# Kernel tuning notes

Hardware: AMD Instinct MI355X
Metric: run time of the kernel (lower is better)

## Reference

```python
import jax, jax.numpy as jnp
import numpy as np

N = 50000            # nodes
E = 800000           # random edges (self loops added in reference, per PyG default)
D_IN, D1, D2, D_OUT = 256, 128, 64, 40
SLOPE = 0.2          # GATv2Conv default negative_slope


def _glorot(key, shape):
    fan_in, fan_out = shape[0], shape[-1]
    s = jnp.sqrt(6.0 / (fan_in + fan_out))
    return jax.random.uniform(key, shape, jnp.float32, -s, s)


def setup_inputs() -> dict:
    key = jax.random.key(0)
    ks = jax.random.split(key, 16)
    inp = {
        "x": jax.random.normal(ks[0], (N, D_IN), jnp.float32),
        "edge_index": jax.random.randint(ks[1], (2, E), 0, N),
    }
    dims = [(D_IN, D1), (D1, D2), (D2, D_OUT)]
    k = 2
    for i, (di, do) in enumerate(dims, 1):
        inp[f"W{i}l"] = _glorot(ks[k], (di, do)); k += 1
        inp[f"W{i}r"] = _glorot(ks[k], (di, do)); k += 1
        inp[f"b{i}l"] = jnp.zeros((do,), jnp.float32)
        inp[f"b{i}r"] = jnp.zeros((do,), jnp.float32)
        inp[f"a{i}"]  = _glorot(ks[k], (do,));    k += 1
        inp[f"c{i}"]  = jnp.zeros((do,), jnp.float32)
    return inp


def _gatv2(x, src, dst, Wl, bl, Wr, br, att, bias):
    # GATv2Conv, heads=1: lin_l on source nodes, lin_r on target nodes
    xl = x @ Wl + bl                     # [N, do] source transform
    xr = x @ Wr + br                     # [N, do] target transform
    e = jax.nn.leaky_relu(xl[src] + xr[dst], SLOPE)   # [Etot, do]
    logits = e @ att                     # [Etot]
    # segment softmax over incoming edges of each dst node
    m = jax.ops.segment_max(logits, dst, num_segments=N)
    ex = jnp.exp(logits - m[dst])
    denom = jax.ops.segment_sum(ex, dst, num_segments=N)
    alpha = ex / denom[dst]              # [Etot]
    out = jax.ops.segment_sum(alpha[:, None] * xl[src], dst, num_segments=N)
    return out + bias


def reference(x, edge_index,
              W1l, W1r, b1l, b1r, a1, c1,
              W2l, W2r, b2l, b2r, a2, c2,
              W3l, W3r, b3l, b3r, a3, c3):
    loop = jnp.arange(N, dtype=edge_index.dtype)
    src = jnp.concatenate([edge_index[0], loop])   # add_self_loops=True
    dst = jnp.concatenate([edge_index[1], loop])
    h = jax.nn.relu(_gatv2(x, src, dst, W1l, b1l, W1r, b1r, a1, c1))
    h = jax.nn.relu(_gatv2(h, src, dst, W2l, b2l, W2r, b2r, a2, c2))
    h = _gatv2(h, src, dst, W3l, b3l, W3r, b3r, a3, c3)
    return jax.nn.log_softmax(h, axis=1)
```

## Files before the change

### kernel.cpp

```cpp
#include <hip/hip_runtime.h>
#include <math.h>

#define NN 50000
#define NE 800000
#define SLOPE 0.2f
#define NEGX (-1e30f)
#define CH 8192

typedef _Float16 h8 __attribute__((ext_vector_type(8)));
typedef _Float16 h2 __attribute__((ext_vector_type(2)));
typedef float f8 __attribute__((ext_vector_type(8)));
typedef float v4f __attribute__((ext_vector_type(4)));

__device__ __forceinline__ h8 hzero(){ h8 z = {0,0,0,0,0,0,0,0}; return z; }
__device__ __forceinline__ f8 fzero(){ f8 z = {0,0,0,0,0,0,0,0}; return z; }

__device__ __forceinline__ void pack_one(const float* __restrict__ W,
                                         _Float16* __restrict__ Wp,
                                         int DO, int K, int NT, int t){
  int KC = K >> 5;
  if (t >= NT * KC * 64) return;
  int lane = t & 63;
  int rest = t >> 6;
  int c  = rest % KC;
  int nt = rest / KC;
  int col = nt * 16 + (lane & 15);
  int k0  = c * 32 + ((lane >> 4) << 3);
  _Float16 o[8];
#pragma unroll
  for (int j = 0; j < 8; j++){
    float v = (col < DO) ? W[(k0 + j) * DO + col] : 0.f;
    o[j] = (_Float16)v;
  }
  *(ulonglong2*)(Wp + (size_t)t * 8) = *(ulonglong2*)o;
}

__global__ __launch_bounds__(256) void k_pack_hist(
    const float* W1l, const float* W1r, const float* W2l,
    const float* W2r, const float* W3l, const float* W3r,
    _Float16* p1l, _Float16* p1r, _Float16* p2l,
    _Float16* p2r, _Float16* p3l, _Float16* p3r,
    const int* __restrict__ ei, int* __restrict__ gbp){
  __shared__ int h[256];
  int b = blockIdx.x, t = threadIdx.x;
  if (b < 44){
    if      (b < 16) pack_one(W1l, p1l, 128, 256, 8, (b     ) * 256 + t);
    else if (b < 32) pack_one(W1r, p1r, 128, 256, 8, (b - 16) * 256 + t);
    else if (b < 36) pack_one(W2l, p2l,  64, 128, 4, (b - 32) * 256 + t);
    else if (b < 40) pack_one(W2r, p2r,  64, 128, 4, (b - 36) * 256 + t);
    else if (b < 42) pack_one(W3l, p3l,  40,  64, 3, (b - 40) * 256 + t);
    else             pack_one(W3r, p3r,  40,  64, 3, (b - 42) * 256 + t);
  } else {
    int hb = b - 44;
    h[t] = 0;
    __syncthreads();
    int e0 = hb * 12500;
    for (int i = t; i < 12500; i += 256)
      atomicAdd(&h[ei[NE + e0 + i] >> 8], 1);
    __syncthreads();
    gbp[hb * 256 + t] = h[t];
  }
}

__global__ __launch_bounds__(256) void k_scan(const int* __restrict__ gbp,
                                              int* __restrict__ base,
                                              int* __restrict__ bcur,
                                              int* __restrict__ row_ptr){
  __shared__ int s[256];
  int t = threadIdx.x;
  int v = 0;
#pragma unroll 8
  for (int i = 0; i < 64; i++) v += gbp[i * 256 + t];
  s[t] = v; __syncthreads();
  for (int off = 1; off < 256; off <<= 1){
    int a = (t >= off) ? s[t - off] : 0;
    __syncthreads(); s[t] += a; __syncthreads();
  }
  int ex = s[t] - v;
  base[t] = ex;
  bcur[t] = ex;
  if (t == 255){ base[256] = s[255]; row_ptr[NN] = s[255]; }
}

__global__ __launch_bounds__(256) void k_bscatter(const int* __restrict__ ei,
                                                  int* __restrict__ bcur,
                                                  unsigned* __restrict__ pk_out){
  __shared__ unsigned pk[CH];
  __shared__ int h[256];
  int t = threadIdx.x;
  int e0 = blockIdx.x * CH;
  h[t] = 0;
  __syncthreads();
  int n = NE - e0; if (n > CH) n = CH;
  for (int i = t; i < n; i += 256){
    int e = e0 + i;
    int s = ei[e], d = ei[NE + e];
    pk[i] = (unsigned)s | ((unsigned)(d & 255) << 16) | ((unsigned)(d >> 8) << 24);
    atomicAdd(&h[d >> 8], 1);
  }
  __syncthreads();
  int c = h[t];
  if (c) h[t] = atomicAdd(&bcur[t], c);
  __syncthreads();
  for (int i = t; i < n; i += 256){
    unsigned u = pk[i];
    int pos = atomicAdd(&h[u >> 24], 1);
    pk_out[pos] = u;
  }
}

__global__ __launch_bounds__(256) void k_bcsr(const unsigned* __restrict__ pk,
                                              const int* __restrict__ base,
                                              int* __restrict__ row_ptr,
                                              int* __restrict__ csr_src){
  __shared__ int h[256], s[256];
  int t = threadIdx.x;
  int b = blockIdx.x;
  int lo = base[b], hi = base[b + 1];
  h[t] = 0;
  __syncthreads();
  for (int i = lo + t; i < hi; i += 256)
    atomicAdd(&h[(pk[i] >> 16) & 255], 1);
  __syncthreads();
  int v = h[t];
  s[t] = v; __syncthreads();
  for (int off = 1; off < 256; off <<= 1){
    int a = (t >= off) ? s[t - off] : 0;
    __syncthreads(); s[t] += a; __syncthreads();
  }
  int ex = lo + s[t] - v;
  int node = b * 256 + t;
  if (node < NN) row_ptr[node] = ex;
  h[t] = ex;
  __syncthreads();
  for (int i = lo + t; i < hi; i += 256){
    unsigned u = pk[i];
    int pos = atomicAdd(&h[(u >> 16) & 255], 1);
    csr_src[pos] = (int)(u & 0xFFFFu);
  }
}

template<typename TI, int K, int DO>
__global__ __launch_bounds__(256, 4) void gemm_direct(
    const TI* __restrict__ X,
    const _Float16* __restrict__ Wpl, const float* __restrict__ bl,
    const _Float16* __restrict__ Wpr, const float* __restrict__ br,
    _Float16* __restrict__ Yl, _Float16* __restrict__ Yr)
{
  constexpr int KC = K / 32;
  constexpr int NT = (DO + 15) / 16;
  int lane = threadIdx.x & 63;
  int wv   = threadIdx.x >> 6;
  int row0 = (blockIdx.x * 4 + wv) * 16;
  int arow = lane & 15;
  int koff = lane >> 4;
  int lrow = row0 + arow;
  int crow = (lrow < NN) ? lrow : 0;

  h8 afrag[KC];
  if constexpr (sizeof(TI) == 4){
    const float* Xr = (const float*)X + (size_t)crow * K + koff * 8;
#pragma unroll
    for (int c = 0; c < KC; c++){
      float4 v0 = *reinterpret_cast<const float4*>(Xr + c * 32);
      float4 v1 = *reinterpret_cast<const float4*>(Xr + c * 32 + 4);
      h8 a;
      a[0]=(_Float16)v0.x; a[1]=(_Float16)v0.y; a[2]=(_Float16)v0.z; a[3]=(_Float16)v0.w;
      a[4]=(_Float16)v1.x; a[5]=(_Float16)v1.y; a[6]=(_Float16)v1.z; a[7]=(_Float16)v1.w;
      afrag[c] = a;
    }
  } else {
    const _Float16* Xr = (const _Float16*)X + (size_t)crow * K + koff * 8;
#pragma unroll
    for (int c = 0; c < KC; c++)
      afrag[c] = *reinterpret_cast<const h8*>(Xr + c * 32);
  }

#pragma unroll
  for (int side = 0; side < 2; side++){
    const _Float16* Wp = side ? Wpr : Wpl;
    const float* bias = side ? br : bl;
    _Float16* Y = side ? Yr : Yl;
#pragma unroll
    for (int nt = 0; nt < NT; nt++){
      v4f acc = {0.f, 0.f, 0.f, 0.f};
#pragma unroll
      for (int c = 0; c < KC; c++){
        h8 b = *reinterpret_cast<const h8*>(Wp + (size_t)((nt * KC + c) * 64 + lane) * 8);
        acc = __builtin_amdgcn_mfma_f32_16x16x32_f16(afrag[c], b, acc, 0, 0, 0);
      }
      int col = nt * 16 + arow;
      if (col < DO){
        float bv = bias[col];
        int rbase = row0 + koff * 4;
#pragma unroll
        for (int r = 0; r < 4; r++){
          int orow = rbase + r;
          if (orow < NN) Y[(size_t)orow * DO + col] = (_Float16)(acc[r] + bv);
        }
      }
    }
  }
}

__device__ __forceinline__ float edge_logit(h8 x, h8 xrv, h8 attv){
  h8 t = x + xrv;
  h8 l = __builtin_elementwise_max(t, t * (_Float16)SLOPE);
  const h2* lp = (const h2*)&l;
  const h2* ap = (const h2*)&attv;
  h2 d = lp[0] * ap[0];
  d += lp[1] * ap[1];
  d += lp[2] * ap[2];
  d += lp[3] * ap[3];
  return (float)d[0] + (float)d[1];
}

template<int LPG>
__device__ __forceinline__ float gsum(float v){
#pragma unroll
  for (int off = 1; off < LPG; off <<= 1) v += __shfl_xor(v, off, 64);
  return v;
}
template<int LPG>
__device__ __forceinline__ void gsum2(float& a, float& b){
#pragma unroll
  for (int off = 1; off < LPG; off <<= 1){
    a += __shfl_xor(a, off, 64);
    b += __shfl_xor(b, off, 64);
  }
}
template<int LPG>
__device__ __forceinline__ void gsum4(float& a, float& b, float& c, float& d){
#pragma unroll
  for (int off = 1; off < LPG; off <<= 1){
    a += __shfl_xor(a, off, 64);
    b += __shfl_xor(b, off, 64);
    c += __shfl_xor(c, off, 64);
    d += __shfl_xor(d, off, 64);
  }
}
template<int LPG>
__device__ __forceinline__ float gmax(float v){
#pragma unroll
  for (int off = 1; off < LPG; off <<= 1) v = fmaxf(v, __shfl_xor(v, off, 64));
  return v;
}

template<int DO, int LPG, int DO2>
__global__ __launch_bounds__(256) void agg_gemm(
    const _Float16* __restrict__ xl, const _Float16* __restrict__ xr,
    const int* __restrict__ csr_src, const int* __restrict__ row_ptr,
    const float* __restrict__ att, const float* __restrict__ bias,
    const _Float16* __restrict__ Wpl2, const float* __restrict__ bl2,
    const _Float16* __restrict__ Wpr2, const float* __restrict__ br2,
    _Float16* __restrict__ Yl, _Float16* __restrict__ Yr)
{
  constexpr int G = 64 / LPG;
  constexpr int NPB = 4 * G;
  constexpr int LK = DO + 8;
  constexpr int KC2 = DO / 32;
  constexpr int NT2 = (DO2 + 15) / 16;
  constexpr int MT = NPB / 16;
  __shared__ _Float16 hs[NPB * LK];
  __shared__ int nodeOf[NPB];
  __shared__ int degOf[NPB];

  int tid  = threadIdx.x;
  int lane = tid & 63;
  int wid  = tid >> 6;

  if (tid < NPB){
    int nd = blockIdx.x * NPB + tid;
    degOf[tid] = (nd < NN) ? (row_ptr[nd + 1] - row_ptr[nd]) : -1;
  }
  __syncthreads();
  if (tid < NPB){
    int dg = degOf[tid];
    int r = 0;
#pragma unroll
    for (int j = 0; j < NPB; j++){
      int dj = degOf[j];
      r += (dj < dg) || (dj == dg && j < tid);
    }
    nodeOf[r] = blockIdx.x * NPB + tid;
  }
  __syncthreads();

  int g = lane / LPG, p = lane % LPG;
  int nodeLocal = wid * G + g;
  int node = nodeOf[nodeLocal];
  int cbase = p * 8;
  bool nvalid = node < NN;
  int nodeC = nvalid ? node : 0;

  h8 attv, xrv, xlv;
  {
    float4 a0 = *reinterpret_cast<const float4*>(att + cbase);
    float4 a1 = *reinterpret_cast<const float4*>(att + cbase + 4);
    attv[0]=(_Float16)a0.x; attv[1]=(_Float16)a0.y; attv[2]=(_Float16)a0.z; attv[3]=(_Float16)a0.w;
    attv[4]=(_Float16)a1.x; attv[5]=(_Float16)a1.y; attv[6]=(_Float16)a1.z; attv[7]=(_Float16)a1.w;
    xrv = *reinterpret_cast<const h8*>(xr + nodeC * DO + cbase);
    xlv = *reinterpret_cast<const h8*>(xl + nodeC * DO + cbase);
  }
  float s = gsum<LPG>(edge_logit(xlv, xrv, attv));
  float wS = __expf(s);
  float denA = wS, denB = 0.f;
  f8 accA, accB;
  {
    f8 xf = __builtin_convertvector(xlv, f8);
    accA = xf * wS;
    accB = fzero();
  }

  int e0 = row_ptr[nodeC];
  int e1 = nvalid ? row_ptr[nodeC + 1] : e0;
  int e = e0;
  for (; e + 3 < e1; e += 4){
    int s0 = csr_src[e],     s1 = csr_src[e + 1];
    int s2 = csr_src[e + 2], s3 = csr_src[e + 3];
    h8 x0 = *reinterpret_cast<const h8*>(xl + s0 * DO + cbase);
    h8 x1 = *reinterpret_cast<const h8*>(xl + s1 * DO + cbase);
    h8 x2 = *reinterpret_cast<const h8*>(xl + s2 * DO + cbase);
    h8 x3 = *reinterpret_cast<const h8*>(xl + s3 * DO + cbase);
    float p0 = edge_logit(x0, xrv, attv);
    float p1 = edge_logit(x1, xrv, attv);
    float p2 = edge_logit(x2, xrv, attv);
    float p3 = edge_logit(x3, xrv, attv);
    gsum4<LPG>(p0, p1, p2, p3);
    float w0 = __expf(p0), w1 = __expf(p1);
    float w2 = __expf(p2), w3 = __expf(p3);
    denA += w0 + w2; denB += w1 + w3;
    accA = __builtin_convertvector(x0, f8) * w0 + accA;
    accB = __builtin_convertvector(x1, f8) * w1 + accB;
    accA = __builtin_convertvector(x2, f8) * w2 + accA;
    accB = __builtin_convertvector(x3, f8) * w3 + accB;
  }
  for (; e + 1 < e1; e += 2){
    int sA = csr_src[e], sB = csr_src[e + 1];
    h8 xA = *reinterpret_cast<const h8*>(xl + sA * DO + cbase);
    h8 xB = *reinterpret_cast<const h8*>(xl + sB * DO + cbase);
    float pA = edge_logit(xA, xrv, attv);
    float pB = edge_logit(xB, xrv, attv);
    gsum2<LPG>(pA, pB);
    float wA = __expf(pA), wB = __expf(pB);
    denA += wA; denB += wB;
    accA = __builtin_convertvector(xA, f8) * wA + accA;
    accB = __builtin_convertvector(xB, f8) * wB + accB;
  }
  if (e < e1){
    int sA = csr_src[e];
    h8 xA = *reinterpret_cast<const h8*>(xl + sA * DO + cbase);
    float pA = gsum<LPG>(edge_logit(xA, xrv, attv));
    float w = __expf(pA);
    denA += w;
    accA = __builtin_convertvector(xA, f8) * w + accA;
  }

  {
    float inv = 1.0f / (denA + denB);
    f8 sum = (accA + accB) * inv;
    float4 b0 = *reinterpret_cast<const float4*>(bias + cbase);
    float4 b1 = *reinterpret_cast<const float4*>(bias + cbase + 4);
    f8 bv = {b0.x, b0.y, b0.z, b0.w, b1.x, b1.y, b1.z, b1.w};
    sum += bv;
    sum = __builtin_elementwise_max(sum, fzero());
    *reinterpret_cast<h8*>(&hs[nodeLocal * LK + cbase]) = __builtin_convertvector(sum, h8);
  }
  __syncthreads();

  int arow = lane & 15;
  int koff = lane >> 4;
  int mt = (MT == 1) ? 0 : (wid >> 1);
  h8 afrag[KC2];
#pragma unroll
  for (int c = 0; c < KC2; c++)
    afrag[c] = *reinterpret_cast<const h8*>(&hs[(mt * 16 + arow) * LK + koff * 8 + c * 32]);

  int side = wid & 1;
  const _Float16* Wp = side ? Wpr2 : Wpl2;
  const float* bias2 = side ? br2 : bl2;
  _Float16* Y = side ? Yr : Yl;
  int nt_begin = (MT == 1) ? (wid >> 1) * (NT2 / 2) : 0;
  int nt_end   = (MT == 1) ? nt_begin + NT2 / 2 : NT2;
  for (int nt = nt_begin; nt < nt_end; nt++){
    v4f acc = {0.f, 0.f, 0.f, 0.f};
#pragma unroll
    for (int c = 0; c < KC2; c++){
      h8 b = *reinterpret_cast<const h8*>(Wp + (size_t)((nt * KC2 + c) * 64 + lane) * 8);
      acc = __builtin_amdgcn_mfma_f32_16x16x32_f16(afrag[c], b, acc, 0, 0, 0);
    }
    int col = nt * 16 + arow;
    if (col < DO2){
      float bv = bias2[col];
      int lrbase = mt * 16 + koff * 4;
#pragma unroll
      for (int r = 0; r < 4; r++){
        int orow = nodeOf[lrbase + r];
        if (orow < NN) Y[(size_t)orow * DO2 + col] = (_Float16)(acc[r] + bv);
      }
    }
  }
}

template<int DO, int LPG>
__global__ __launch_bounds__(256) void gat_agg_out(
    const _Float16* __restrict__ xl, const _Float16* __restrict__ xr,
    const int* __restrict__ csr_src, const int* __restrict__ row_ptr,
    const float* __restrict__ att, const float* __restrict__ bias,
    float* __restrict__ out)
{
  constexpr int G = 64 / LPG;
  constexpr int NPB = 4 * G;
  __shared__ int nodeOf[NPB];
  __shared__ int degOf[NPB];
  int tid  = threadIdx.x;
  int lane = tid & 63;
  int wid  = tid >> 6;

  if (tid < NPB){
    int nd = blockIdx.x * NPB + tid;
    degOf[tid] = (nd < NN) ? (row_ptr[nd + 1] - row_ptr[nd]) : -1;
  }
  __syncthreads();
  if (tid < NPB){
    int dg = degOf[tid];
    int r = 0;
#pragma unroll
    for (int j = 0; j < NPB; j++){
      int dj = degOf[j];
      r += (dj < dg) || (dj == dg && j < tid);
    }
    nodeOf[r] = blockIdx.x * NPB + tid;
  }
  __syncthreads();

  int g = lane / LPG;
  int p = lane % LPG;
  int node = nodeOf[wid * G + g];
  bool nvalid = node < NN;
  int nodeC = nvalid ? node : 0;
  int cbase = p * 8;
  bool ok = (cbase < DO);

  h8 attv = hzero(), xrv = hzero(), xlv = hzero();
  if (ok){
    float4 a0 = *reinterpret_cast<const float4*>(att + cbase);
    float4 a1 = *reinterpret_cast<const float4*>(att + cbase + 4);
    attv[0]=(_Float16)a0.x; attv[1]=(_Float16)a0.y; attv[2]=(_Float16)a0.z; attv[3]=(_Float16)a0.w;
    attv[4]=(_Float16)a1.x; attv[5]=(_Float16)a1.y; attv[6]=(_Float16)a1.z; attv[7]=(_Float16)a1.w;
    xrv = *reinterpret_cast<const h8*>(xr + nodeC * DO + cbase);
    xlv = *reinterpret_cast<const h8*>(xl + nodeC * DO + cbase);
  }

  float s = gsum<LPG>(edge_logit(xlv, xrv, attv));
  float wS = __expf(s);
  float denA = wS, denB = 0.f;
  f8 accA, accB;
  {
    f8 xf = __builtin_convertvector(xlv, f8);
    accA = xf * wS;
    accB = fzero();
  }

  int e0 = row_ptr[nodeC];
  int e1 = nvalid ? row_ptr[nodeC + 1] : e0;
  int e = e0;
  for (; e + 3 < e1; e += 4){
    int s0 = csr_src[e],     s1 = csr_src[e + 1];
    int s2 = csr_src[e + 2], s3 = csr_src[e + 3];
    h8 x0 = ok ? *reinterpret_cast<const h8*>(xl + s0 * DO + cbase) : hzero();
    h8 x1 = ok ? *reinterpret_cast<const h8*>(xl + s1 * DO + cbase) : hzero();
    h8 x2 = ok ? *reinterpret_cast<const h8*>(xl + s2 * DO + cbase) : hzero();
    h8 x3 = ok ? *reinterpret_cast<const h8*>(xl + s3 * DO + cbase) : hzero();
    float p0 = edge_logit(x0, xrv, attv);
    float p1 = edge_logit(x1, xrv, attv);
    float p2 = edge_logit(x2, xrv, attv);
    float p3 = edge_logit(x3, xrv, attv);
    gsum4<LPG>(p0, p1, p2, p3);
    float w0 = __expf(p0), w1 = __expf(p1);
    float w2 = __expf(p2), w3 = __expf(p3);
    denA += w0 + w2; denB += w1 + w3;
    accA = __builtin_convertvector(x0, f8) * w0 + accA;
    accB = __builtin_convertvector(x1, f8) * w1 + accB;
    accA = __builtin_convertvector(x2, f8) * w2 + accA;
    accB = __builtin_convertvector(x3, f8) * w3 + accB;
  }
  for (; e + 1 < e1; e += 2){
    int sA = csr_src[e], sB = csr_src[e + 1];
    h8 xA = ok ? *reinterpret_cast<const h8*>(xl + sA * DO + cbase) : hzero();
    h8 xB = ok ? *reinterpret_cast<const h8*>(xl + sB * DO + cbase) : hzero();
    float pA = edge_logit(xA, xrv, attv);
    float pB = edge_logit(xB, xrv, attv);
    gsum2<LPG>(pA, pB);
    float wA = __expf(pA), wB = __expf(pB);
    denA += wA; denB += wB;
    accA = __builtin_convertvector(xA, f8) * wA + accA;
    accB = __builtin_convertvector(xB, f8) * wB + accB;
  }
  if (e < e1){
    int sA = csr_src[e];
    h8 xA = ok ? *reinterpret_cast<const h8*>(xl + sA * DO + cbase) : hzero();
    float pA = gsum<LPG>(edge_logit(xA, xrv, attv));
    float w = __expf(pA);
    denA += w;
    accA = __builtin_convertvector(xA, f8) * w + accA;
  }

  float inv = 1.0f / (denA + denB);
  f8 sumv = (accA + accB) * inv;
  float v[8]; float lmax = NEGX;
#pragma unroll
  for (int j = 0; j < 8; j++){
    v[j] = ok ? (sumv[j] + bias[cbase + j]) : NEGX;
    lmax = fmaxf(lmax, v[j]);
  }
  lmax = gmax<LPG>(lmax);
  float lsum = 0.f;
#pragma unroll
  for (int j = 0; j < 8; j++) lsum += __expf(v[j] - lmax);
  lsum = gsum<LPG>(lsum);
  if (ok && nvalid){
    float lg = lmax + __logf(lsum);
    float* op = (float*)out + node * DO + cbase;
    float4 o0, o1;
    o0.x = v[0] - lg; o0.y = v[1] - lg; o0.z = v[2] - lg; o0.w = v[3] - lg;
    o1.x = v[4] - lg; o1.y = v[5] - lg; o1.z = v[6] - lg; o1.w = v[7] - lg;
    *reinterpret_cast<float4*>(op) = o0;
    *reinterpret_cast<float4*>(op + 4) = o1;
  }
}

extern "C" void kernel_launch(void* const* d_in, const int* in_sizes, int n_in,
                              void* d_out, int out_size, void* d_ws, size_t ws_size,
                              hipStream_t stream) {
  const float* x   = (const float*)d_in[0];
  const int*   ei  = (const int*)d_in[1];
  const float* W1l = (const float*)d_in[2];  const float* W1r = (const float*)d_in[3];
  const float* b1l = (const float*)d_in[4];  const float* b1r = (const float*)d_in[5];
  const float* a1  = (const float*)d_in[6];  const float* c1  = (const float*)d_in[7];
  const float* W2l = (const float*)d_in[8];  const float* W2r = (const float*)d_in[9];
  const float* b2l = (const float*)d_in[10]; const float* b2r = (const float*)d_in[11];
  const float* a2  = (const float*)d_in[12]; const float* c2  = (const float*)d_in[13];
  const float* W3l = (const float*)d_in[14]; const float* W3r = (const float*)d_in[15];
  const float* b3l = (const float*)d_in[16]; const float* b3r = (const float*)d_in[17];
  const float* a3  = (const float*)d_in[18]; const float* c3  = (const float*)d_in[19];
  float* outp = (float*)d_out;

  _Float16* xl1 = (_Float16*)d_ws;
  _Float16* xr1 = xl1 + 6400000;
  _Float16* xl2 = xr1 + 6400000;
  _Float16* xr2 = xl2 + 3200000;
  _Float16* xl3 = xr2 + 3200000;
  _Float16* xr3 = xl3 + 2000000;
  _Float16* wp1l = xr3 + 2000000;
  _Float16* wp1r = wp1l + 32768;
  _Float16* wp2l = wp1r + 32768;
  _Float16* wp2r = wp2l + 8192;
  _Float16* wp3l = wp2r + 8192;
  _Float16* wp3r = wp3l + 3072;
  unsigned* pk   = (unsigned*)(wp3r + 3072);
  int* csr_src   = (int*)(pk + NE);
  int* row_ptr   = csr_src + NE;
  int* gbp       = row_ptr + 50001;
  int* base      = gbp + 16384;
  int* bcur      = base + 257;

  const int GB = (NN + 63) / 64;
  const int SB = (NE + CH - 1) / CH;
  const int FB1 = (NN + 15) / 16;
  const int FB2 = (NN + 31) / 32;
  const int AB3 = (NN + 31) / 32;

  k_pack_hist<<<108, 256, 0, stream>>>(W1l, W1r, W2l, W2r, W3l, W3r,
                                       wp1l, wp1r, wp2l, wp2r, wp3l, wp3r,
                                       ei, gbp);
  k_scan<<<1, 256, 0, stream>>>(gbp, base, bcur, row_ptr);
  k_bscatter<<<SB, 256, 0, stream>>>(ei, bcur, pk);
  k_bcsr<<<196, 256, 0, stream>>>(pk, base, row_ptr, csr_src);

  gemm_direct<float,256,128><<<GB, 256, 0, stream>>>(x, wp1l, b1l, wp1r, b1r, xl1, xr1);

  agg_gemm<128,16,64><<<FB1, 256, 0, stream>>>(xl1, xr1, csr_src, row_ptr,
                                               a1, c1, wp2l, b2l, wp2r, b2r, xl2, xr2);

  agg_gemm<64,8,40><<<FB2, 256, 0, stream>>>(xl2, xr2, csr_src, row_ptr,
                                             a2, c2, wp3l, b3l, wp3r, b3r, xl3, xr3);

  gat_agg_out<40,8><<<AB3, 256, 0, stream>>>(xl3, xr3, csr_src, row_ptr, a3, c3, outp);
}
```

Baseline: 290.1 us.

## Sort nodes globally by degree and feed aggregation blocks from the permutation

The CSR build now also histograms node in-degrees (capped at 255) and runs an extra scan and scatter to produce a global degree-sorted node permutation. The aggregation kernels take their node lists from contiguous slices of this permutation, chosen through a scrambled block index, instead of sorting degrees inside each block. The goal is for groups within a wave and across blocks to have nearly equal edge counts, which cuts divergence and tail imbalance. In exchange it adds two kernel launches and loses the contiguous node locality for the self-row reads. The 4-edge unrolled loop is also removed, leaving only the 2-edge loop, which lowers register pressure but gives up some load-level parallelism.

```diff
diff --git a/kernel.cpp b/kernel.cpp
--- a/kernel.cpp
+++ b/kernel.cpp
@@ -65,9 +65,11 @@
 __global__ __launch_bounds__(256) void k_scan(const int* __restrict__ gbp,
                                               int* __restrict__ base,
                                               int* __restrict__ bcur,
-                                              int* __restrict__ row_ptr){
+                                              int* __restrict__ row_ptr,
+                                              int* __restrict__ dcnt){
   __shared__ int s[256];
   int t = threadIdx.x;
+  dcnt[t] = 0;
   int v = 0;
 #pragma unroll 8
   for (int i = 0; i < 64; i++) v += gbp[i * 256 + t];
@@ -112,7 +114,8 @@
 __global__ __launch_bounds__(256) void k_bcsr(const unsigned* __restrict__ pk,
                                               const int* __restrict__ base,
                                               int* __restrict__ row_ptr,
-                                              int* __restrict__ csr_src){
+                                              int* __restrict__ csr_src,
+                                              int* __restrict__ dcnt){
   __shared__ int h[256], s[256];
   int t = threadIdx.x;
   int b = blockIdx.x;
@@ -132,11 +135,54 @@
   int node = b * 256 + t;
   if (node < NN) row_ptr[node] = ex;
   h[t] = ex;
-  __syncthreads();
+  s[t] = 0;
+  __syncthreads();
+  if (node < NN) atomicAdd(&s[v < 255 ? v : 255], 1);
+  __syncthreads();
+  if (s[t]) atomicAdd(&dcnt[t], s[t]);
   for (int i = lo + t; i < hi; i += 256){
     unsigned u = pk[i];
     int pos = atomicAdd(&h[(u >> 16) & 255], 1);
     csr_src[pos] = (int)(u & 0xFFFFu);
+  }
+}
+
+__global__ __launch_bounds__(256) void k_dscan(const int* __restrict__ dcnt,
+                                               int* __restrict__ dcur){
+  __shared__ int s[256];
+  int t = threadIdx.x;
+  int v = dcnt[t];
+  s[t] = v; __syncthreads();
+  for (int off = 1; off < 256; off <<= 1){
+    int a = (t >= off) ? s[t - off] : 0;
+    __syncthreads(); s[t] += a; __syncthreads();
+  }
+  dcur[t] = s[t] - v;
+}
+
+__global__ __launch_bounds__(256) void k_dscatter(const int* __restrict__ row_ptr,
+                                                  int* __restrict__ dcur,
+                                                  int* __restrict__ perm){
+  __shared__ int lh[256];
+  int t = threadIdx.x;
+  int node = blockIdx.x * 256 + t;
+  lh[t] = 0;
+  __syncthreads();
+  int bin = -1;
+  if (node < NN){
+    int deg = row_ptr[node + 1] - row_ptr[node];
+    bin = deg < 255 ? deg : 255;
+    atomicAdd(&lh[bin], 1);
+  }
+  __syncthreads();
+  int c = lh[t];
+  int bp = c ? atomicAdd(&dcur[t], c) : 0;
+  __syncthreads();
+  lh[t] = bp;
+  __syncthreads();
+  if (node < NN){
+    int pos = atomicAdd(&lh[bin], 1);
+    perm[pos] = node;
   }
 }
 
@@ -230,16 +276,6 @@
   }
 }
 template<int LPG>
-__device__ __forceinline__ void gsum4(float& a, float& b, float& c, float& d){
-#pragma unroll
-  for (int off = 1; off < LPG; off <<= 1){
-    a += __shfl_xor(a, off, 64);
-    b += __shfl_xor(b, off, 64);
-    c += __shfl_xor(c, off, 64);
-    d += __shfl_xor(d, off, 64);
-  }
-}
-template<int LPG>
 __device__ __forceinline__ float gmax(float v){
 #pragma unroll
   for (int off = 1; off < LPG; off <<= 1) v = fmaxf(v, __shfl_xor(v, off, 64));
@@ -250,6 +286,7 @@
 __global__ __launch_bounds__(256) void agg_gemm(
     const _Float16* __restrict__ xl, const _Float16* __restrict__ xr,
     const int* __restrict__ csr_src, const int* __restrict__ row_ptr,
+    const int* __restrict__ perm,
     const float* __restrict__ att, const float* __restrict__ bias,
     const _Float16* __restrict__ Wpl2, const float* __restrict__ bl2,
     const _Float16* __restrict__ Wpr2, const float* __restrict__ br2,
@@ -263,26 +300,15 @@
   constexpr int MT = NPB / 16;
   __shared__ _Float16 hs[NPB * LK];
   __shared__ int nodeOf[NPB];
-  __shared__ int degOf[NPB];
 
   int tid  = threadIdx.x;
   int lane = tid & 63;
   int wid  = tid >> 6;
 
+  unsigned seg = (unsigned)(blockIdx.x * 1021u) % gridDim.x;
   if (tid < NPB){
-    int nd = blockIdx.x * NPB + tid;
-    degOf[tid] = (nd < NN) ? (row_ptr[nd + 1] - row_ptr[nd]) : -1;
-  }
-  __syncthreads();
-  if (tid < NPB){
-    int dg = degOf[tid];
-    int r = 0;
-#pragma unroll
-    for (int j = 0; j < NPB; j++){
-      int dj = degOf[j];
-      r += (dj < dg) || (dj == dg && j < tid);
-    }
-    nodeOf[r] = blockIdx.x * NPB + tid;
+    int idx = seg * NPB + tid;
+    nodeOf[tid] = (idx < NN) ? perm[idx] : NN;
   }
   __syncthreads();
 
@@ -315,26 +341,6 @@
   int e0 = row_ptr[nodeC];
   int e1 = nvalid ? row_ptr[nodeC + 1] : e0;
   int e = e0;
-  for (; e + 3 < e1; e += 4){
-    int s0 = csr_src[e],     s1 = csr_src[e + 1];
-    int s2 = csr_src[e + 2], s3 = csr_src[e + 3];
-    h8 x0 = *reinterpret_cast<const h8*>(xl + s0 * DO + cbase);
-    h8 x1 = *reinterpret_cast<const h8*>(xl + s1 * DO + cbase);
-    h8 x2 = *reinterpret_cast<const h8*>(xl + s2 * DO + cbase);
-    h8 x3 = *reinterpret_cast<const h8*>(xl + s3 * DO + cbase);
-    float p0 = edge_logit(x0, xrv, attv);
-    float p1 = edge_logit(x1, xrv, attv);
-    float p2 = edge_logit(x2, xrv, attv);
-    float p3 = edge_logit(x3, xrv, attv);
-    gsum4<LPG>(p0, p1, p2, p3);
-    float w0 = __expf(p0), w1 = __expf(p1);
-    float w2 = __expf(p2), w3 = __expf(p3);
-    denA += w0 + w2; denB += w1 + w3;
-    accA = __builtin_convertvector(x0, f8) * w0 + accA;
-    accB = __builtin_convertvector(x1, f8) * w1 + accB;
-    accA = __builtin_convertvector(x2, f8) * w2 + accA;
-    accB = __builtin_convertvector(x3, f8) * w3 + accB;
-  }
   for (; e + 1 < e1; e += 2){
     int sA = csr_src[e], sB = csr_src[e + 1];
     h8 xA = *reinterpret_cast<const h8*>(xl + sA * DO + cbase);
@@ -406,31 +412,21 @@
 __global__ __launch_bounds__(256) void gat_agg_out(
     const _Float16* __restrict__ xl, const _Float16* __restrict__ xr,
     const int* __restrict__ csr_src, const int* __restrict__ row_ptr,
+    const int* __restrict__ perm,
     const float* __restrict__ att, const float* __restrict__ bias,
     float* __restrict__ out)
 {
   constexpr int G = 64 / LPG;
   constexpr int NPB = 4 * G;
   __shared__ int nodeOf[NPB];
-  __shared__ int degOf[NPB];
   int tid  = threadIdx.x;
   int lane = tid & 63;
   int wid  = tid >> 6;
 
+  unsigned seg = (unsigned)(blockIdx.x * 1021u) % gridDim.x;
   if (tid < NPB){
-    int nd = blockIdx.x * NPB + tid;
-    degOf[tid] = (nd < NN) ? (row_ptr[nd + 1] - row_ptr[nd]) : -1;
-  }
-  __syncthreads();
-  if (tid < NPB){
-    int dg = degOf[tid];
-    int r = 0;
-#pragma unroll
-    for (int j = 0; j < NPB; j++){
-      int dj = degOf[j];
-      r += (dj < dg) || (dj == dg && j < tid);
-    }
-    nodeOf[r] = blockIdx.x * NPB + tid;
+    int idx = seg * NPB + tid;
+    nodeOf[tid] = (idx < NN) ? perm[idx] : NN;
   }
   __syncthreads();
 
@@ -465,26 +461,6 @@
   int e0 = row_ptr[nodeC];
   int e1 = nvalid ? row_ptr[nodeC + 1] : e0;
   int e = e0;
-  for (; e + 3 < e1; e += 4){
-    int s0 = csr_src[e],     s1 = csr_src[e + 1];
-    int s2 = csr_src[e + 2], s3 = csr_src[e + 3];
-    h8 x0 = ok ? *reinterpret_cast<const h8*>(xl + s0 * DO + cbase) : hzero();
-    h8 x1 = ok ? *reinterpret_cast<const h8*>(xl + s1 * DO + cbase) : hzero();
-    h8 x2 = ok ? *reinterpret_cast<const h8*>(xl + s2 * DO + cbase) : hzero();
-    h8 x3 = ok ? *reinterpret_cast<const h8*>(xl + s3 * DO + cbase) : hzero();
-    float p0 = edge_logit(x0, xrv, attv);
-    float p1 = edge_logit(x1, xrv, attv);
-    float p2 = edge_logit(x2, xrv, attv);
-    float p3 = edge_logit(x3, xrv, attv);
-    gsum4<LPG>(p0, p1, p2, p3);
-    float w0 = __expf(p0), w1 = __expf(p1);
-    float w2 = __expf(p2), w3 = __expf(p3);
-    denA += w0 + w2; denB += w1 + w3;
-    accA = __builtin_convertvector(x0, f8) * w0 + accA;
-    accB = __builtin_convertvector(x1, f8) * w1 + accB;
-    accA = __builtin_convertvector(x2, f8) * w2 + accA;
-    accB = __builtin_convertvector(x3, f8) * w3 + accB;
-  }
   for (; e + 1 < e1; e += 2){
     int sA = csr_src[e], sB = csr_src[e + 1];
     h8 xA = ok ? *reinterpret_cast<const h8*>(xl + sA * DO + cbase) : hzero();
@@ -564,6 +540,9 @@
   int* gbp       = row_ptr + 50001;
   int* base      = gbp + 16384;
   int* bcur      = base + 257;
+  int* perm      = bcur + 256;
+  int* dcnt      = perm + NN;
+  int* dcur      = dcnt + 256;
 
   const int GB = (NN + 63) / 64;
   const int SB = (NE + CH - 1) / CH;
@@ -574,17 +553,19 @@
   k_pack_hist<<<108, 256, 0, stream>>>(W1l, W1r, W2l, W2r, W3l, W3r,
                                        wp1l, wp1r, wp2l, wp2r, wp3l, wp3r,
                                        ei, gbp);
-  k_scan<<<1, 256, 0, stream>>>(gbp, base, bcur, row_ptr);
+  k_scan<<<1, 256, 0, stream>>>(gbp, base, bcur, row_ptr, dcnt);
   k_bscatter<<<SB, 256, 0, stream>>>(ei, bcur, pk);
-  k_bcsr<<<196, 256, 0, stream>>>(pk, base, row_ptr, csr_src);
+  k_bcsr<<<196, 256, 0, stream>>>(pk, base, row_ptr, csr_src, dcnt);
+  k_dscan<<<1, 256, 0, stream>>>(dcnt, dcur);
+  k_dscatter<<<196, 256, 0, stream>>>(row_ptr, dcur, perm);
 
   gemm_direct<float,256,128><<<GB, 256, 0, stream>>>(x, wp1l, b1l, wp1r, b1r, xl1, xr1);
 
-  agg_gemm<128,16,64><<<FB1, 256, 0, stream>>>(xl1, xr1, csr_src, row_ptr,
+  agg_gemm<128,16,64><<<FB1, 256, 0, stream>>>(xl1, xr1, csr_src, row_ptr, perm,
                                                a1, c1, wp2l, b2l, wp2r, b2r, xl2, xr2);
 
-  agg_gemm<64,8,40><<<FB2, 256, 0, stream>>>(xl2, xr2, csr_src, row_ptr,
+  agg_gemm<64,8,40><<<FB2, 256, 0, stream>>>(xl2, xr2, csr_src, row_ptr, perm,
                                              a2, c2, wp3l, b3l, wp3r, b3r, xl3, xr3);
 
-  gat_agg_out<40,8><<<AB3, 256, 0, stream>>>(xl3, xr3, csr_src, row_ptr, a3, c3, outp);
-}
+  gat_agg_out<40,8><<<AB3, 256, 0, stream>>>(xl3, xr3, csr_src, row_ptr, perm, a3, c3, outp);
+}
```

After: 291.5 us. Within noise of the previous version (+0.5%).
